# Kernel optimization log

Measured on AMD Instinct MI355X. Metric: run time of the kernel, lower is better.

Reference implementation:

```python
import jax, jax.numpy as jnp
import numpy as np

B, S, H, G, W_LOC = 2, 4096, 12, 64, 513  # Longformer-base: window=2*256+1, 64 global slots


def setup_inputs() -> dict:
    key = jax.random.key(0)
    k1, = jax.random.split(key, 1)
    attention_probs = jax.random.uniform(k1, (B, S, H, G + W_LOC), dtype=jnp.float32)
    attention_mask = jnp.zeros((B, S), dtype=jnp.float32)  # all tokens currently kept
    # global tokens are the first G positions of every batch; nonzero(as_tuple) index arrays
    b_idx = jnp.repeat(jnp.arange(B, dtype=jnp.int64), G)
    g_idx = jnp.tile(jnp.arange(G, dtype=jnp.int64), B)
    return {
        "attention_mask": attention_mask,
        "attention_probs": attention_probs,
        "keep_threshold": jnp.asarray(0.005, dtype=jnp.float32),  # base 0.01*6/12 + learned 0
        "max_num_global_attn_indices": G,
        "loc_b": b_idx, "loc_i": g_idx,
        "glob_b": b_idx, "glob_i": g_idx,
    }


def reference(attention_mask, attention_probs, keep_threshold,
              max_num_global_attn_indices, loc_b, loc_i, glob_b, glob_i):
    Gn = max_num_global_attn_indices
    b, s, h, wg = attention_probs.shape
    w = wg - Gn  # local window size, odd
    half = w // 2

    # zero out rows of already-masked tokens (attention_mask < 0)
    probs = jnp.where((attention_mask < 0)[:, :, None, None], 0.0, attention_probs)

    gl = probs[..., :Gn]                              # [B,S,H,G]
    lo = jnp.transpose(probs[..., Gn:], (0, 2, 1, 3))  # [B,H,S,W]

    # anti-diagonal (key-column) sums of the local band; equals the source's
    # conv2d-with-flipped-identity + slice: out[j] = sum_c lo[j + half - c, c]
    lo_p = jnp.pad(lo, ((0, 0), (0, 0), (half, half), (0, 0)))  # [B,H,S+W-1,W]
    rows = jnp.arange(s)[:, None] + (w - 1) - jnp.arange(w)[None, :]  # [S,W]
    diag = lo_p[:, :, rows, jnp.arange(w)[None, :]]  # [B,H,S,W]
    local_sum = diag.sum(axis=(1, 3))                # [B,S] (summed over heads too)

    global_sum = gl.sum(axis=(1, 2))                 # [B,G]
    probs_sum = local_sum.at[loc_b, loc_i].add(global_sum[glob_b, glob_i])

    probs_max = probs_sum.max(axis=-1, keepdims=True)
    scores = probs_sum / probs_max

    thr = jnp.maximum(jnp.float32(1e-5), jnp.asarray(keep_threshold, jnp.float32).reshape(()))
    new_attention_mask = jnp.where(scores < thr, jnp.float32(-10000.0), jnp.float32(0.0))
    return new_attention_mask, scores
```

## Files before the change

### kernel.cpp

```cpp
#include <hip/hip_runtime.h>
#include <float.h>

#define Bsz 2
#define Ssz 4096
#define Hsz 12
#define Gsz 64
#define Wsz 513
#define Csz (Gsz + Wsz)
#define ROW (Hsz * Csz)
#define HALF 256
#define RPB 8
#define WIN (RPB + Wsz - 1)

#define PSUM_SZ ((size_t)Bsz * Ssz)
#define GACC_SZ ((size_t)Bsz * Gsz)

__global__ __launch_bounds__(256) void k1_fused(
    const float* __restrict__ probs, const float* __restrict__ mask,
    float* __restrict__ psum, float* __restrict__ gacc)
{
    __shared__ float lds[ROW];
    __shared__ float win[WIN];
    const int t = threadIdx.x;
    const int row0 = blockIdx.x * RPB;
    const int b = row0 / Ssz;
    float g = 0.f;

    for (int w = t; w < WIN; w += 256) win[w] = 0.f;

    for (int r = 0; r < RPB; ++r) {
        const int row = row0 + r;
        const float4* src = (const float4*)(probs + (size_t)row * ROW);
        float4* dst = (float4*)lds;
        #pragma unroll
        for (int idx = t; idx < ROW / 4; idx += 256) dst[idx] = src[idx];
        __syncthreads();

        const float scale = (mask[row] < 0.f) ? 0.f : 1.f;
        for (int c = t; c < Csz; c += 256) {
            float v = 0.f;
            #pragma unroll
            for (int h = 0; h < Hsz; ++h) v += lds[h * Csz + c];
            v *= scale;
            if (c < Gsz) g += v;
            else win[r + (c - Gsz)] += v;
        }
        __syncthreads();
    }

    const int i_base = (row0 - b * Ssz) - HALF;
    for (int w = t; w < WIN; w += 256) {
        const int i = i_base + w;
        if (i >= 0 && i < Ssz) atomicAdd(&psum[b * Ssz + i], win[w]);
    }
    if (t < Gsz) atomicAdd(&gacc[b * Gsz + t], g);
}

__global__ void k3_scatter(const int* __restrict__ loc_b, const int* __restrict__ loc_i,
                           const int* __restrict__ glob_b, const int* __restrict__ glob_i,
                           const float* __restrict__ gacc, float* __restrict__ psum, int n)
{
    int k = blockIdx.x * blockDim.x + threadIdx.x;
    if (k < n)
        atomicAdd(&psum[loc_b[k] * Ssz + loc_i[k]], gacc[glob_b[k] * Gsz + glob_i[k]]);
}

__global__ __launch_bounds__(1024) void k4_final(
    const float* __restrict__ psum, const float* __restrict__ thr_p,
    float* __restrict__ out)
{
    const int b = blockIdx.x;
    const int t = threadIdx.x;
    const float* p = psum + (size_t)b * Ssz;

    float m = -FLT_MAX;
    for (int i = t; i < Ssz; i += 1024) m = fmaxf(m, p[i]);
    #pragma unroll
    for (int off = 32; off >= 1; off >>= 1) m = fmaxf(m, __shfl_down(m, off, 64));

    __shared__ float red[16];
    const int wave = t >> 6, lane = t & 63;
    if (lane == 0) red[wave] = m;
    __syncthreads();
    if (t == 0) {
        float mm = red[0];
        #pragma unroll
        for (int w = 1; w < 16; ++w) mm = fmaxf(mm, red[w]);
        red[0] = mm;
    }
    __syncthreads();
    const float mx = red[0];
    const float thr = fmaxf(1e-5f, thr_p[0]);

    for (int i = t; i < Ssz; i += 1024) {
        float sc = p[i] / mx;
        out[(size_t)Bsz * Ssz + (size_t)b * Ssz + i] = sc;
        out[(size_t)b * Ssz + i] = (sc < thr) ? -10000.f : 0.f;
    }
}

extern "C" void kernel_launch(void* const* d_in, const int* in_sizes, int n_in,
                              void* d_out, int out_size, void* d_ws, size_t ws_size,
                              hipStream_t stream)
{
    const float* mask  = (const float*)d_in[0];
    const float* probs = (const float*)d_in[1];
    const float* thr   = (const float*)d_in[2];
    const int* loc_b  = (const int*)d_in[4];
    const int* loc_i  = (const int*)d_in[5];
    const int* glob_b = (const int*)d_in[6];
    const int* glob_i = (const int*)d_in[7];
    const int n_idx = in_sizes[4];

    float* psum = (float*)d_ws;
    float* gacc = psum + PSUM_SZ;
    float* out  = (float*)d_out;

    hipMemsetAsync(psum, 0, (PSUM_SZ + GACC_SZ) * sizeof(float), stream);

    k1_fused<<<dim3(Bsz * Ssz / RPB), dim3(256), 0, stream>>>(probs, mask, psum, gacc);
    k3_scatter<<<dim3(1), dim3(128), 0, stream>>>(loc_b, loc_i, glob_b, glob_i, gacc, psum, n_idx);
    k4_final<<<dim3(Bsz), dim3(1024), 0, stream>>>(psum, thr, out);
}
```

Before: 333.4 us.

## Stream head sums directly from global memory and fold scatter into final kernel

The main kernel no longer stages each row into LDS with a barrier. Each thread sums its three columns across heads using nontemporal global loads, then adds into the window buffer with LDS atomics. Occupancy hints are added via launch bounds. The separate scatter kernel is removed and its global-slot additions are done in shared memory inside the final normalization kernel, saving one launch at the cost of a 16KB LDS copy per batch.

```diff
diff --git a/kernel.cpp b/kernel.cpp
--- a/kernel.cpp
+++ b/kernel.cpp
@@ -15,11 +15,10 @@
 #define PSUM_SZ ((size_t)Bsz * Ssz)
 #define GACC_SZ ((size_t)Bsz * Gsz)
 
-__global__ __launch_bounds__(256) void k1_fused(
+__global__ __launch_bounds__(256, 4) void k1_fused(
     const float* __restrict__ probs, const float* __restrict__ mask,
     float* __restrict__ psum, float* __restrict__ gacc)
 {
-    __shared__ float lds[ROW];
     __shared__ float win[WIN];
     const int t = threadIdx.x;
     const int row0 = blockIdx.x * RPB;
@@ -27,26 +26,31 @@
     float g = 0.f;
 
     for (int w = t; w < WIN; w += 256) win[w] = 0.f;
+    __syncthreads();
 
     for (int r = 0; r < RPB; ++r) {
         const int row = row0 + r;
-        const float4* src = (const float4*)(probs + (size_t)row * ROW);
-        float4* dst = (float4*)lds;
+        const float* base = probs + (size_t)row * ROW;
+        const float scale = (mask[row] < 0.f) ? 0.f : 1.f;
+
+        float v0 = 0.f, v1 = 0.f, v2 = 0.f;
         #pragma unroll
-        for (int idx = t; idx < ROW / 4; idx += 256) dst[idx] = src[idx];
-        __syncthreads();
+        for (int h = 0; h < Hsz; ++h) {
+            const float* hp = base + h * Csz;
+            v0 += __builtin_nontemporal_load(hp + t);
+            v1 += __builtin_nontemporal_load(hp + t + 256);
+            if (t < Csz - 512)
+                v2 += __builtin_nontemporal_load(hp + t + 512);
+        }
+        v0 *= scale; v1 *= scale; v2 *= scale;
 
-        const float scale = (mask[row] < 0.f) ? 0.f : 1.f;
-        for (int c = t; c < Csz; c += 256) {
-            float v = 0.f;
-            #pragma unroll
-            for (int h = 0; h < Hsz; ++h) v += lds[h * Csz + c];
-            v *= scale;
-            if (c < Gsz) g += v;
-            else win[r + (c - Gsz)] += v;
-        }
-        __syncthreads();
+        if (t < Gsz) g += v0;
+        else atomicAdd(&win[(t - Gsz) + r], v0);
+        atomicAdd(&win[(t + 256 - Gsz) + r], v1);
+        if (t < Csz - 512)
+            atomicAdd(&win[(t + 512 - Gsz) + r], v2);
     }
+    __syncthreads();
 
     const int i_base = (row0 - b * Ssz) - HALF;
     for (int w = t; w < WIN; w += 256) {
@@ -56,25 +60,28 @@
     if (t < Gsz) atomicAdd(&gacc[b * Gsz + t], g);
 }
 
-__global__ void k3_scatter(const int* __restrict__ loc_b, const int* __restrict__ loc_i,
-                           const int* __restrict__ glob_b, const int* __restrict__ glob_i,
-                           const float* __restrict__ gacc, float* __restrict__ psum, int n)
-{
-    int k = blockIdx.x * blockDim.x + threadIdx.x;
-    if (k < n)
-        atomicAdd(&psum[loc_b[k] * Ssz + loc_i[k]], gacc[glob_b[k] * Gsz + glob_i[k]]);
-}
-
 __global__ __launch_bounds__(1024) void k4_final(
     const float* __restrict__ psum, const float* __restrict__ thr_p,
+    const int* __restrict__ loc_b, const int* __restrict__ loc_i,
+    const int* __restrict__ glob_b, const int* __restrict__ glob_i,
+    const float* __restrict__ gacc, int n_idx,
     float* __restrict__ out)
 {
     const int b = blockIdx.x;
     const int t = threadIdx.x;
+    __shared__ float sp[Ssz];
     const float* p = psum + (size_t)b * Ssz;
 
+    for (int i = t; i < Ssz; i += 1024) sp[i] = p[i];
+    __syncthreads();
+
+    for (int k = t; k < n_idx; k += 1024)
+        if (loc_b[k] == b)
+            atomicAdd(&sp[loc_i[k]], gacc[glob_b[k] * Gsz + glob_i[k]]);
+    __syncthreads();
+
     float m = -FLT_MAX;
-    for (int i = t; i < Ssz; i += 1024) m = fmaxf(m, p[i]);
+    for (int i = t; i < Ssz; i += 1024) m = fmaxf(m, sp[i]);
     #pragma unroll
     for (int off = 32; off >= 1; off >>= 1) m = fmaxf(m, __shfl_down(m, off, 64));
 
@@ -93,7 +100,7 @@
     const float thr = fmaxf(1e-5f, thr_p[0]);
 
     for (int i = t; i < Ssz; i += 1024) {
-        float sc = p[i] / mx;
+        float sc = sp[i] / mx;
         out[(size_t)Bsz * Ssz + (size_t)b * Ssz + i] = sc;
         out[(size_t)b * Ssz + i] = (sc < thr) ? -10000.f : 0.f;
     }
@@ -119,6 +126,6 @@
     hipMemsetAsync(psum, 0, (PSUM_SZ + GACC_SZ) * sizeof(float), stream);
 
     k1_fused<<<dim3(Bsz * Ssz / RPB), dim3(256), 0, stream>>>(probs, mask, psum, gacc);
-    k3_scatter<<<dim3(1), dim3(128), 0, stream>>>(loc_b, loc_i, glob_b, glob_i, gacc, psum, n_idx);
-    k4_final<<<dim3(Bsz), dim3(1024), 0, stream>>>(psum, thr, out);
+    k4_final<<<dim3(Bsz), dim3(1024), 0, stream>>>(psum, thr, loc_b, loc_i,
+                                                   glob_b, glob_i, gacc, n_idx, out);
 }
```

Result: slower. 344.4 us (+3.3%).
